# Kernel optimization log

Hardware: AMD Instinct MI355X
Metric: run time of the kernel (lower is better)

## Reference

```python
import jax, jax.numpy as jnp
import numpy as np

B, S, D = 2, 2048, 2048
H, HKV, DH = 16, 4, 128   # query heads, kv heads, head dim
N_REP = H // HKV
ROPE_BASE = 10000.0


def rotate_half(x):
    x1, x2 = x[..., : DH // 2], x[..., DH // 2 :]
    return jnp.concatenate((-x2, x1), axis=-1)


def rope_tables(seq_len, dtype=jnp.float32):
    inv_freq = 1.0 / (ROPE_BASE ** (jnp.arange(0, DH, 2, dtype=jnp.float32) / DH))
    t = jnp.arange(seq_len, dtype=jnp.float32)
    freqs = jnp.outer(t, inv_freq)                 # [S, DH/2]
    emb = jnp.concatenate((freqs, freqs), axis=-1)  # [S, DH]
    return jnp.cos(emb).astype(dtype), jnp.sin(emb).astype(dtype)


def setup_inputs() -> dict:
    key = jax.random.key(0)
    k1, k2, k3, k4, k5 = jax.random.split(key, 5)
    scale = 1.0 / np.sqrt(D)
    return {
        "hidden_states": jax.random.normal(k1, (B, S, D), dtype=jnp.float32),
        "position_ids": jnp.tile(jnp.arange(S, dtype=jnp.int32)[None, :], (B, 1)),
        "wq": jax.random.normal(k2, (D, H * DH), dtype=jnp.float32) * scale,
        "wk": jax.random.normal(k3, (D, HKV * DH), dtype=jnp.float32) * scale,
        "wv": jax.random.normal(k4, (D, HKV * DH), dtype=jnp.float32) * scale,
        "wo": jax.random.normal(k5, (H * DH, D), dtype=jnp.float32) * scale,
    }


def reference(hidden_states, position_ids, wq, wk, wv, wo):
    x = hidden_states
    b, s, _ = x.shape

    # QKV projections -> [B, H(kv), S, DH]
    q = (x @ wq).reshape(b, s, H, DH).transpose(0, 2, 1, 3)
    k = (x @ wk).reshape(b, s, HKV, DH).transpose(0, 2, 1, 3)
    v = (x @ wv).reshape(b, s, HKV, DH).transpose(0, 2, 1, 3)

    # Rotary position embedding
    cos_t, sin_t = rope_tables(s, x.dtype)
    cos = cos_t[position_ids][:, None, :, :]  # [B,1,S,DH]
    sin = sin_t[position_ids][:, None, :, :]
    q = q * cos + rotate_half(q) * sin
    k = k * cos + rotate_half(k) * sin

    # GQA: repeat KV heads to match query heads
    k = jnp.repeat(k, N_REP, axis=1)  # [B,H,S,DH]
    v = jnp.repeat(v, N_REP, axis=1)

    # Causal SDPA
    scores = jnp.einsum("bhqd,bhkd->bhqk", q, k) / jnp.sqrt(
        jnp.asarray(DH, x.dtype)
    )
    causal = jnp.tril(jnp.ones((s, s), dtype=bool))
    scores = jnp.where(causal[None, None], scores, jnp.asarray(-1e9, x.dtype))
    attn = jax.nn.softmax(scores, axis=-1)
    out = jnp.einsum("bhqk,bhkd->bhqd", attn, v)  # [B,H,S,DH]

    out = out.transpose(0, 2, 1, 3).reshape(b, s, H * DH)
    return out @ wo
```

## Files before the change

### kernel.cpp

```cpp
#include <hip/hip_runtime.h>
#include <cmath>

typedef unsigned short u16;
typedef float floatx4 __attribute__((ext_vector_type(4)));
typedef short short8 __attribute__((ext_vector_type(8)));
typedef short short4v __attribute__((ext_vector_type(4)));
typedef __bf16 bf16x8 __attribute__((ext_vector_type(8)));

#define GLOBAL_AS __attribute__((address_space(1)))
#define LDS_AS __attribute__((address_space(3)))

#define S_LEN 2048
#define D_MODEL 2048
#define NH 16
#define NKV 4
#define DHEAD 128
#define SM_SCALE 0.08838834764831843f
#define K2 (SM_SCALE * 1.4426950408889634f)

__device__ __forceinline__ u16 f2bf(float f) {
    unsigned int u = __builtin_bit_cast(unsigned int, f);
    u += 0x7fffu + ((u >> 16) & 1u);
    return (u16)(u >> 16);
}
__device__ __forceinline__ u16 f2bfr(float f) {
    unsigned int u = __builtin_bit_cast(unsigned int, f);
    return (u16)((u + 0x8000u) >> 16);
}
__device__ __forceinline__ float bf2f(u16 x) {
    unsigned int u = ((unsigned int)x) << 16;
    return __builtin_bit_cast(float, u);
}
__device__ __forceinline__ floatx4 zf4() {
    floatx4 z; z[0] = 0.f; z[1] = 0.f; z[2] = 0.f; z[3] = 0.f; return z;
}
__device__ __forceinline__ floatx4 mfma16(short8 a, short8 b, floatx4 c) {
    return __builtin_amdgcn_mfma_f32_16x16x32_bf16(
        __builtin_bit_cast(bf16x8, a), __builtin_bit_cast(bf16x8, b), c, 0, 0, 0);
}
__device__ __forceinline__ floatx4 mfma16k16(short4v a, short4v b, floatx4 c) {
    return __builtin_amdgcn_mfma_f32_16x16x16bf16_1k(a, b, c, 0, 0, 0);
}
__device__ __forceinline__ void async16(const u16* g, u16* l) {
    __builtin_amdgcn_global_load_lds((GLOBAL_AS void*)g, (LDS_AS void*)l, 16, 0, 0);
}

__global__ void cast_tables_kernel(const float4* __restrict__ in, ushort4* __restrict__ out,
                                   float* __restrict__ cs_tab, float* __restrict__ sn_tab) {
    int bid = blockIdx.x;
    if (bid < 8192) {
        int i = bid * 256 + threadIdx.x;
        float4 v = in[i];
        ushort4 o;
        o.x = f2bf(v.x); o.y = f2bf(v.y); o.z = f2bf(v.z); o.w = f2bf(v.w);
        out[i] = o;
    } else {
        int idx = (bid - 8192) * 256 + threadIdx.x;
        int p = idx >> 6, jj = idx & 63;
        double e = (double)(2 * jj) / 128.0;
        double invf = pow(10000.0, -e);
        float arg = (float)p * (float)invf;
        cs_tab[idx] = (float)cos((double)arg);
        sn_tab[idx] = (float)sin((double)arg);
    }
}

__global__ void transpose_all_kernel(const float* __restrict__ wq, const float* __restrict__ wk,
                                     const float* __restrict__ wv, const float* __restrict__ wo,
                                     u16* __restrict__ Wqkv, u16* __restrict__ Wo) {
    __shared__ float tile[32][33];
    int x = blockIdx.x;
    const float* in; u16* out; int C, bx;
    if (x < 64)      { in = wq; out = Wqkv;                     C = 2048; bx = x * 32; }
    else if (x < 80) { in = wk; out = Wqkv + (size_t)2048*2048; C = 512;  bx = (x - 64) * 32; }
    else if (x < 96) { in = wv; out = Wqkv + (size_t)2560*2048; C = 512;  bx = (x - 80) * 32; }
    else             { in = wo; out = Wo;                       C = 2048; bx = (x - 96) * 32; }
    const int R = 2048;
    int tx = threadIdx.x & 31, ty = threadIdx.x >> 5;
    int by = blockIdx.y * 32;
#pragma unroll
    for (int i = 0; i < 32; i += 8)
        tile[ty + i][tx] = in[(size_t)(by + ty + i) * C + bx + tx];
    __syncthreads();
#pragma unroll
    for (int i = 0; i < 32; i += 8)
        out[(size_t)(bx + ty + i) * R + by + tx] = f2bf(tile[tx][ty + i]);
}

__global__ void rope_k_kernel(u16* __restrict__ Kb, const int* __restrict__ pos,
                              const float4* __restrict__ cs_tab,
                              const float4* __restrict__ sn_tab) {
    int idx = blockIdx.x * 256 + threadIdx.x;
    int j4 = idx & 15;
    int s = (idx >> 4) & 2047;
    int r = idx >> 15;
    int hh = r & 3, b = r >> 2;
    int p = pos[b * S_LEN + s];
    float4 cs = cs_tab[p * 16 + j4];
    float4 sn = sn_tab[p * 16 + j4];
    u16* base = Kb + (((size_t)(b * NKV + hh)) * S_LEN + s) * DHEAD + j4 * 4;
    ushort4 a = *(const ushort4*)(base);
    ushort4 c = *(const ushort4*)(base + 64);
    ushort4 oa, oc;
    float x1, x2;
    x1 = bf2f(a.x); x2 = bf2f(c.x); oa.x = f2bf(x1 * cs.x - x2 * sn.x); oc.x = f2bf(x2 * cs.x + x1 * sn.x);
    x1 = bf2f(a.y); x2 = bf2f(c.y); oa.y = f2bf(x1 * cs.y - x2 * sn.y); oc.y = f2bf(x2 * cs.y + x1 * sn.y);
    x1 = bf2f(a.z); x2 = bf2f(c.z); oa.z = f2bf(x1 * cs.z - x2 * sn.z); oc.z = f2bf(x2 * cs.z + x1 * sn.z);
    x1 = bf2f(a.w); x2 = bf2f(c.w); oa.w = f2bf(x1 * cs.w - x2 * sn.w); oc.w = f2bf(x2 * cs.w + x1 * sn.w);
    *(ushort4*)(base) = oa;
    *(ushort4*)(base + 64) = oc;
}

template <int M_REP>
__device__ __forceinline__ void gemm_8ph(const u16* __restrict__ A,
                                         const u16* __restrict__ Bt, int K,
                                         u16* ldsA, u16* ldsB,
                                         floatx4 acc[M_REP][4]) {
    constexpr int BM = M_REP * 32;
    constexpr int ALOADS = BM / 64;
    const int t = threadIdx.x;
    const int lane = t & 63, wave = t >> 6;
    const int wr = wave >> 2, wc = wave & 3;
    const int lr = lane & 15, q = lane >> 4;
    const int swz = lr & 7;
    const int m0 = blockIdx.y * BM, n0 = blockIdx.x * 256;

#pragma unroll
    for (int r = 0; r < M_REP; ++r)
#pragma unroll
        for (int c = 0; c < 4; ++c) acc[r][c] = zf4();

    auto stageT = [&](int kt, int bs) {
#pragma unroll
        for (int i = 0; i < ALOADS; ++i) {
            int ci = i * 512 + t;
            int grow = ci >> 3;
            int kc = ((ci & 7) ^ (grow & 7)) << 3;
            async16(A + (size_t)(m0 + grow) * K + kt * 64 + kc,
                    ldsA + bs * (BM * 64) + (i * 512 + wave * 64) * 8);
        }
#pragma unroll
        for (int i = 0; i < 4; ++i) {
            int ci = i * 512 + t;
            int grow = ci >> 3;
            int kc = ((ci & 7) ^ (grow & 7)) << 3;
            async16(Bt + (size_t)(n0 + grow) * K + kt * 64 + kc,
                    ldsB + bs * (256 * 64) + (i * 512 + wave * 64) * 8);
        }
    };

    const int NT = K / 64;
    stageT(0, 0);

    for (int kt = 0; kt < NT; ++kt) {
        const int cur = kt & 1, nxt = cur ^ 1;
        const int kn = (kt + 1 < NT) ? kt + 1 : 0;
        const u16* la = ldsA + cur * (BM * 64);
        const u16* lb = ldsB + cur * (256 * 64);
        short8 af[M_REP / 2][2], bf[4][2];

        stageT(kn, nxt);
        if constexpr (M_REP == 8) asm volatile("s_waitcnt vmcnt(8)" ::: "memory");
        else                      asm volatile("s_waitcnt vmcnt(6)" ::: "memory");
        __builtin_amdgcn_s_barrier();
#pragma unroll
        for (int nf = 0; nf < 2; ++nf)
#pragma unroll
            for (int ks = 0; ks < 2; ++ks)
                bf[nf][ks] = *(const short8*)(lb + (wc * 64 + nf * 16 + lr) * 64 +
                                              (((ks * 4 + q) ^ swz) << 3));
#pragma unroll
        for (int mf = 0; mf < M_REP / 2; ++mf)
#pragma unroll
            for (int ks = 0; ks < 2; ++ks)
                af[mf][ks] = *(const short8*)(la + (wr * (M_REP * 16) + mf * 16 + lr) * 64 +
                                              (((ks * 4 + q) ^ swz) << 3));
        __builtin_amdgcn_s_barrier();
        __builtin_amdgcn_s_setprio(1);
#pragma unroll
        for (int mf = 0; mf < M_REP / 2; ++mf)
#pragma unroll
            for (int nf = 0; nf < 2; ++nf)
#pragma unroll
                for (int ks = 0; ks < 2; ++ks)
                    acc[mf][nf] = mfma16(af[mf][ks], bf[nf][ks], acc[mf][nf]);
        __builtin_amdgcn_s_setprio(0);
        __builtin_amdgcn_s_barrier();

#pragma unroll
        for (int nf = 0; nf < 2; ++nf)
#pragma unroll
            for (int ks = 0; ks < 2; ++ks)
                bf[2 + nf][ks] = *(const short8*)(lb + (wc * 64 + (2 + nf) * 16 + lr) * 64 +
                                                  (((ks * 4 + q) ^ swz) << 3));
        __builtin_amdgcn_s_barrier();
        __builtin_amdgcn_s_setprio(1);
#pragma unroll
        for (int mf = 0; mf < M_REP / 2; ++mf)
#pragma unroll
            for (int nf = 2; nf < 4; ++nf)
#pragma unroll
                for (int ks = 0; ks < 2; ++ks)
                    acc[mf][nf] = mfma16(af[mf][ks], bf[nf][ks], acc[mf][nf]);
        __builtin_amdgcn_s_setprio(0);
        __builtin_amdgcn_s_barrier();

#pragma unroll
        for (int mf = 0; mf < M_REP / 2; ++mf)
#pragma unroll
            for (int ks = 0; ks < 2; ++ks)
                af[mf][ks] = *(const short8*)(la + (wr * (M_REP * 16) +
                                              (M_REP / 2 + mf) * 16 + lr) * 64 +
                                              (((ks * 4 + q) ^ swz) << 3));
        __builtin_amdgcn_s_barrier();
        __builtin_amdgcn_s_setprio(1);
#pragma unroll
        for (int mf = 0; mf < M_REP / 2; ++mf)
#pragma unroll
            for (int nf = 0; nf < 2; ++nf)
#pragma unroll
                for (int ks = 0; ks < 2; ++ks)
                    acc[M_REP / 2 + mf][nf] =
                        mfma16(af[mf][ks], bf[nf][ks], acc[M_REP / 2 + mf][nf]);
        __builtin_amdgcn_s_setprio(0);
        __builtin_amdgcn_s_barrier();

        __builtin_amdgcn_s_setprio(1);
#pragma unroll
        for (int mf = 0; mf < M_REP / 2; ++mf)
#pragma unroll
            for (int nf = 2; nf < 4; ++nf)
#pragma unroll
                for (int ks = 0; ks < 2; ++ks)
                    acc[M_REP / 2 + mf][nf] =
                        mfma16(af[mf][ks], bf[nf][ks], acc[M_REP / 2 + mf][nf]);
        __builtin_amdgcn_s_setprio(0);
        __builtin_amdgcn_s_barrier();
    }
    asm volatile("s_waitcnt vmcnt(0)" ::: "memory");
}

__global__ __launch_bounds__(512, 1) void qkv_gemm_kernel(const u16* __restrict__ A,
                                                          const u16* __restrict__ Bt,
                                                          u16* __restrict__ Qb,
                                                          u16* __restrict__ Kb,
                                                          u16* __restrict__ Vt) {
    __shared__ u16 ldsA[2 * 256 * 64];
    __shared__ u16 ldsB[2 * 256 * 64];
    floatx4 acc[8][4];
    gemm_8ph<8>(A, Bt, D_MODEL, ldsA, ldsB, acc);

    const int t = threadIdx.x, lane = t & 63, wave = t >> 6;
    const int wr = wave >> 2, wc = wave & 3, lr = lane & 15, q = lane >> 4;
    const int m0 = blockIdx.y * 256 + wr * 128, n0 = blockIdx.x * 256 + wc * 64;
#pragma unroll
    for (int r = 0; r < 8; ++r)
#pragma unroll
        for (int c = 0; c < 4; ++c) {
            int gc = n0 + c * 16 + lr;
#pragma unroll
            for (int rr = 0; rr < 4; ++rr) {
                int grow = m0 + r * 16 + q * 4 + rr;
                int bb = grow >> 11, s = grow & 2047;
                u16 bv = f2bf(acc[r][c][rr]);
                int d = gc & 127;
                if (gc < 2048) {
                    int hh = gc >> 7;
                    Qb[(((size_t)(bb * NH + hh)) * S_LEN + s) * DHEAD + d] = bv;
                } else if (gc < 2560) {
                    int hh = (gc - 2048) >> 7;
                    Kb[(((size_t)(bb * NKV + hh)) * S_LEN + s) * DHEAD + d] = bv;
                } else {
                    int hh = (gc - 2560) >> 7;
                    int s2 = s ^ ((d & 8) >> 1);
                    Vt[(((size_t)(bb * NKV + hh)) * DHEAD + d) * S_LEN + s2] = bv;
                }
            }
        }
}

__global__ __launch_bounds__(512, 1) void out_gemm_kernel(const u16* __restrict__ A,
                                                          const u16* __restrict__ Bt,
                                                          float* __restrict__ out) {
    __shared__ u16 ldsA[2 * 128 * 64];
    __shared__ u16 ldsB[2 * 256 * 64];
    floatx4 acc[4][4];
    gemm_8ph<4>(A, Bt, D_MODEL, ldsA, ldsB, acc);

    const int t = threadIdx.x, lane = t & 63, wave = t >> 6;
    const int wr = wave >> 2, wc = wave & 3, lr = lane & 15, q = lane >> 4;
    const int m0 = blockIdx.y * 128 + wr * 64, n0 = blockIdx.x * 256 + wc * 64;
#pragma unroll
    for (int r = 0; r < 4; ++r)
#pragma unroll
        for (int c = 0; c < 4; ++c) {
            int gc = n0 + c * 16 + lr;
#pragma unroll
            for (int rr = 0; rr < 4; ++rr) {
                int grow = m0 + r * 16 + q * 4 + rr;
                out[(size_t)grow * D_MODEL + gc] = acc[r][c][rr];
            }
        }
}

__global__ __launch_bounds__(256, 2) void fa_kernel(const u16* __restrict__ Qb,
                                                    const u16* __restrict__ Kb,
                                                    const u16* __restrict__ Vt,
                                                    u16* __restrict__ Ob,
                                                    const int* __restrict__ pos,
                                                    const float4* __restrict__ cs_tab,
                                                    const float4* __restrict__ sn_tab) {
    __shared__ u16 ldsK[2][64 * 128];
    __shared__ u16 ldsV[2][128 * 64];

    const int t = threadIdx.x, lane = t & 63, wave = t >> 6;
    const int lr = lane & 15, q = lane >> 4;
    const int swz = lr & 7;

    const int bid = blockIdx.x;
    const int bh = bid >> 4, p = bid & 15;
    const int qt0 = p, qt1 = 31 - p;
    const int b = bh >> 4, h = bh & 15;
    const int kvh = h >> 2;

    const u16* Kp = Kb + (size_t)(b * NKV + kvh) * S_LEN * DHEAD;
    const u16* Vp = Vt + (size_t)(b * NKV + kvh) * DHEAD * S_LEN;

    short8 qf0[4], qf1[4];
    auto load_rope_q = [&](int qt, short8 (&qf)[4]) {
        const u16* Qp = Qb + ((size_t)((b * NH + h) * S_LEN) + qt * 64 + wave * 16) * DHEAD;
#pragma unroll
        for (int kk = 0; kk < 4; ++kk)
            qf[kk] = *(const short8*)(Qp + (size_t)lr * DHEAD + kk * 32 + q * 8);
        const int srow = qt * 64 + wave * 16 + lr;
        const int pp = pos[b * S_LEN + srow];
#pragma unroll
        for (int kk = 0; kk < 2; ++kk)
#pragma unroll
            for (int h4 = 0; h4 < 2; ++h4) {
                float4 cs = cs_tab[pp * 16 + kk * 8 + q * 2 + h4];
                float4 sn = sn_tab[pp * 16 + kk * 8 + q * 2 + h4];
#pragma unroll
                for (int e = 0; e < 4; ++e) {
                    float cc = (&cs.x)[e], ss = (&sn.x)[e];
                    int ei = h4 * 4 + e;
                    float x1 = bf2f((u16)qf[kk][ei]);
                    float x2 = bf2f((u16)qf[kk + 2][ei]);
                    qf[kk][ei]     = (short)f2bf(x1 * cc - x2 * ss);
                    qf[kk + 2][ei] = (short)f2bf(x2 * cc + x1 * ss);
                }
            }
    };
    load_rope_q(qt0, qf0);
    load_rope_q(qt1, qf1);

    auto stage = [&](int kt, int bs) {
#pragma unroll
        for (int i = 0; i < 4; ++i) {
            int ci = i * 256 + t;
            int krow = ci >> 4, kc = ((ci & 15) ^ ((ci >> 4) & 7)) << 3;
            async16(Kp + (size_t)(kt * 64 + krow) * DHEAD + kc,
                    &ldsK[bs][(i * 256 + wave * 64) * 8]);
            int dh = ci >> 3, vc = ((ci & 7) ^ ((ci >> 3) & 7)) << 3;
            async16(Vp + (size_t)dh * S_LEN + kt * 64 + vc,
                    &ldsV[bs][(i * 256 + wave * 64) * 8]);
        }
    };

    floatx4 accO[8];
    float m_i, l_i;

    auto do_tile = [&](int kt, int qt_c, const short8 (&qfc)[4], int bs) {
        floatx4 sc[4];
        __builtin_amdgcn_s_setprio(1);
#pragma unroll
        for (int c = 0; c < 4; ++c) {
            sc[c] = zf4();
#pragma unroll
            for (int kk = 0; kk < 4; ++kk) {
                short8 kfr = *(const short8*)(&ldsK[bs][(c * 16 + lr) * DHEAD +
                                              (((kk * 4 + q) ^ swz) << 3)]);
                sc[c] = mfma16(kfr, qfc[kk], sc[c]);
            }
        }
        __builtin_amdgcn_s_setprio(0);

        if (kt == qt_c) {
            const int qrow = wave * 16 + lr;
#pragma unroll
            for (int c = 0; c < 4; ++c)
#pragma unroll
                for (int rr = 0; rr < 4; ++rr)
                    if (c * 16 + q * 4 + rr > qrow) sc[c][rr] = -3e38f;
        }

        float mx = -3e38f;
#pragma unroll
        for (int c = 0; c < 4; ++c)
#pragma unroll
            for (int rr = 0; rr < 4; ++rr) mx = fmaxf(mx, sc[c][rr]);
        mx = fmaxf(mx, __shfl_xor(mx, 16));
        mx = fmaxf(mx, __shfl_xor(mx, 32));
        float mnew = fmaxf(m_i, mx);
        float mk = mnew * K2;
        bool anyup = __any(mnew > m_i);
        float rs = 0.f;
#pragma unroll
        for (int c = 0; c < 4; ++c)
#pragma unroll
            for (int rr = 0; rr < 4; ++rr) {
                float pe = __builtin_amdgcn_exp2f(fmaf(sc[c][rr], K2, -mk));
                sc[c][rr] = pe;
                rs += pe;
            }
        rs += __shfl_xor(rs, 16);
        rs += __shfl_xor(rs, 32);
        if (anyup) {
            float alpha = __builtin_amdgcn_exp2f(fmaf(m_i, K2, -mk));
            l_i = l_i * alpha + rs;
#pragma unroll
            for (int d = 0; d < 8; ++d) accO[d] *= alpha;
        } else {
            l_i += rs;
        }
        m_i = mnew;

        short4v pb[4];
#pragma unroll
        for (int c = 0; c < 4; ++c) {
            pb[c][0] = (short)f2bfr(sc[c][0]);
            pb[c][1] = (short)f2bfr(sc[c][1]);
            pb[c][2] = (short)f2bfr(sc[c][2]);
            pb[c][3] = (short)f2bfr(sc[c][3]);
        }

        __builtin_amdgcn_s_setprio(1);
#pragma unroll
        for (int ks = 0; ks < 4; ++ks)
#pragma unroll
            for (int d = 0; d < 8; ++d) {
                short4v vf = *(const short4v*)(&ldsV[bs][(d * 16 + lr) * 64 +
                                               (((ks * 2 + (q >> 1)) ^ swz) << 3) +
                                               (((q ^ (lr >> 3)) & 1) << 2)]);
                accO[d] = mfma16k16(vf, pb[ks], accO[d]);
            }
        __builtin_amdgcn_s_setprio(0);
    };

    auto epilogue = [&](int qt_c) {
        const int tok = qt_c * 64 + wave * 16 + lr;
        const float inv = 1.0f / l_i;
        u16* orow = Ob + ((size_t)(b * S_LEN + tok)) * (NH * DHEAD) + h * DHEAD + q * 4;
#pragma unroll
        for (int d = 0; d < 8; ++d) {
            ushort4 o;
            o.x = f2bf(accO[d][0] * inv);
            o.y = f2bf(accO[d][1] * inv);
            o.z = f2bf(accO[d][2] * inv);
            o.w = f2bf(accO[d][3] * inv);
            *(ushort4*)(orow + d * 16) = o;
        }
    };

#pragma unroll
    for (int d = 0; d < 8; ++d) accO[d] = zf4();
    m_i = -3e38f; l_i = 0.f;

    int cur = 0;
    stage(0, 0);
    __syncthreads();

    for (int kt = 0; kt <= qt0; ++kt) {
        int nxt = cur ^ 1;
        int nk = (kt < qt0) ? kt + 1 : 0;
        stage(nk, nxt);
        do_tile(kt, qt0, qf0, cur);
        __syncthreads();
        cur = nxt;
    }
    epilogue(qt0);
#pragma unroll
    for (int d = 0; d < 8; ++d) accO[d] = zf4();
    m_i = -3e38f; l_i = 0.f;

    for (int kt = 0; kt <= qt1; ++kt) {
        int nxt = cur ^ 1;
        if (kt < qt1) stage(kt + 1, nxt);
        do_tile(kt, qt1, qf1, cur);
        __syncthreads();
        cur = nxt;
    }
    epilogue(qt1);
}

extern "C" void kernel_launch(void* const* d_in, const int* in_sizes, int n_in,
                              void* d_out, int out_size, void* d_ws, size_t ws_size,
                              hipStream_t stream) {
    const float* X  = (const float*)d_in[0];
    const int* pos  = (const int*)d_in[1];
    const float* wq = (const float*)d_in[2];
    const float* wk = (const float*)d_in[3];
    const float* wv = (const float*)d_in[4];
    const float* wo = (const float*)d_in[5];
    float* out = (float*)d_out;

    char* w = (char*)d_ws;
    u16* Xbf    = (u16*)(w);
    u16* Wqkv   = (u16*)(w + 16777216);
    u16* Wo     = (u16*)(w + 29360128);
    u16* Qb     = (u16*)(w + 37748736);
    u16* Kb     = (u16*)(w + 54525952);
    u16* Vt     = (u16*)(w + 58720256);
    u16* Ob     = (u16*)(w + 62914560);
    float* cst  = (float*)(w + 79691776);
    float* snt  = (float*)(w + 80216064);

    cast_tables_kernel<<<8704, 256, 0, stream>>>((const float4*)X, (ushort4*)Xbf, cst, snt);
    transpose_all_kernel<<<dim3(160, 64), 256, 0, stream>>>(wq, wk, wv, wo, Wqkv, Wo);
    qkv_gemm_kernel<<<dim3(12, 16), 512, 0, stream>>>(Xbf, Wqkv, Qb, Kb, Vt);
    rope_k_kernel<<<1024, 256, 0, stream>>>(Kb, pos, (const float4*)cst, (const float4*)snt);
    fa_kernel<<<512, 256, 0, stream>>>(Qb, Kb, Vt, Ob, pos, (const float4*)cst, (const float4*)snt);
    out_gemm_kernel<<<dim3(8, 32), 512, 0, stream>>>(Ob, Wo, out);
}
```

Baseline: 340.6 us.

## Fuse prologue kernels, remap GEMM tiles per XCD, restructure small-tile GEMM phases

Merges the input cast/rope-table kernel and the weight transpose kernel into a single prologue launch. Switches the QKV and output GEMMs to 1D grids whose block-to-tile mapping groups tiles sharing A rows onto the same XCD, to improve L2 reuse. For the M_REP=4 GEMM, the inner loop loads all B fragments at once and uses two compute phases instead of four, reducing barriers at the cost of more live registers.

```diff
diff --git a/kernel.cpp b/kernel.cpp
--- a/kernel.cpp
+++ b/kernel.cpp
@@ -45,16 +45,22 @@
     __builtin_amdgcn_global_load_lds((GLOBAL_AS void*)g, (LDS_AS void*)l, 16, 0, 0);
 }
 
-__global__ void cast_tables_kernel(const float4* __restrict__ in, ushort4* __restrict__ out,
-                                   float* __restrict__ cs_tab, float* __restrict__ sn_tab) {
+__global__ void prologue_kernel(const float4* __restrict__ Xin, ushort4* __restrict__ Xout,
+                                float* __restrict__ cs_tab, float* __restrict__ sn_tab,
+                                const float* __restrict__ wq, const float* __restrict__ wk,
+                                const float* __restrict__ wv, const float* __restrict__ wo,
+                                u16* __restrict__ Wqkv, u16* __restrict__ Wo) {
+    __shared__ float tile[32][33];
     int bid = blockIdx.x;
     if (bid < 8192) {
         int i = bid * 256 + threadIdx.x;
-        float4 v = in[i];
+        float4 v = Xin[i];
         ushort4 o;
         o.x = f2bf(v.x); o.y = f2bf(v.y); o.z = f2bf(v.z); o.w = f2bf(v.w);
-        out[i] = o;
-    } else {
+        Xout[i] = o;
+        return;
+    }
+    if (bid < 8704) {
         int idx = (bid - 8192) * 256 + threadIdx.x;
         int p = idx >> 6, jj = idx & 63;
         double e = (double)(2 * jj) / 128.0;
@@ -62,14 +68,10 @@
         float arg = (float)p * (float)invf;
         cs_tab[idx] = (float)cos((double)arg);
         sn_tab[idx] = (float)sin((double)arg);
+        return;
     }
-}
-
-__global__ void transpose_all_kernel(const float* __restrict__ wq, const float* __restrict__ wk,
-                                     const float* __restrict__ wv, const float* __restrict__ wo,
-                                     u16* __restrict__ Wqkv, u16* __restrict__ Wo) {
-    __shared__ float tile[32][33];
-    int x = blockIdx.x;
+    int tb = bid - 8704;
+    int x = tb % 160, y = tb / 160;
     const float* in; u16* out; int C, bx;
     if (x < 64)      { in = wq; out = Wqkv;                     C = 2048; bx = x * 32; }
     else if (x < 80) { in = wk; out = Wqkv + (size_t)2048*2048; C = 512;  bx = (x - 64) * 32; }
@@ -77,7 +79,7 @@
     else             { in = wo; out = Wo;                       C = 2048; bx = (x - 96) * 32; }
     const int R = 2048;
     int tx = threadIdx.x & 31, ty = threadIdx.x >> 5;
-    int by = blockIdx.y * 32;
+    int by = y * 32;
 #pragma unroll
     for (int i = 0; i < 32; i += 8)
         tile[ty + i][tx] = in[(size_t)(by + ty + i) * C + bx + tx];
@@ -112,10 +114,11 @@
 }
 
 template <int M_REP>
-__device__ __forceinline__ void gemm_8ph(const u16* __restrict__ A,
-                                         const u16* __restrict__ Bt, int K,
-                                         u16* ldsA, u16* ldsB,
-                                         floatx4 acc[M_REP][4]) {
+__device__ __forceinline__ void gemm_ph(const u16* __restrict__ A,
+                                        const u16* __restrict__ Bt, int K,
+                                        u16* ldsA, u16* ldsB,
+                                        floatx4 acc[M_REP][4],
+                                        int m0, int n0) {
     constexpr int BM = M_REP * 32;
     constexpr int ALOADS = BM / 64;
     const int t = threadIdx.x;
@@ -123,7 +126,6 @@
     const int wr = wave >> 2, wc = wave & 3;
     const int lr = lane & 15, q = lane >> 4;
     const int swz = lr & 7;
-    const int m0 = blockIdx.y * BM, n0 = blockIdx.x * 256;
 
 #pragma unroll
     for (int r = 0; r < M_REP; ++r)
@@ -157,85 +159,124 @@
         const int kn = (kt + 1 < NT) ? kt + 1 : 0;
         const u16* la = ldsA + cur * (BM * 64);
         const u16* lb = ldsB + cur * (256 * 64);
-        short8 af[M_REP / 2][2], bf[4][2];
 
         stageT(kn, nxt);
         if constexpr (M_REP == 8) asm volatile("s_waitcnt vmcnt(8)" ::: "memory");
         else                      asm volatile("s_waitcnt vmcnt(6)" ::: "memory");
         __builtin_amdgcn_s_barrier();
-#pragma unroll
-        for (int nf = 0; nf < 2; ++nf)
-#pragma unroll
-            for (int ks = 0; ks < 2; ++ks)
-                bf[nf][ks] = *(const short8*)(lb + (wc * 64 + nf * 16 + lr) * 64 +
-                                              (((ks * 4 + q) ^ swz) << 3));
-#pragma unroll
-        for (int mf = 0; mf < M_REP / 2; ++mf)
-#pragma unroll
-            for (int ks = 0; ks < 2; ++ks)
-                af[mf][ks] = *(const short8*)(la + (wr * (M_REP * 16) + mf * 16 + lr) * 64 +
-                                              (((ks * 4 + q) ^ swz) << 3));
-        __builtin_amdgcn_s_barrier();
-        __builtin_amdgcn_s_setprio(1);
-#pragma unroll
-        for (int mf = 0; mf < M_REP / 2; ++mf)
+
+        if constexpr (M_REP == 8) {
+            short8 af[4][2], bf[4][2];
 #pragma unroll
             for (int nf = 0; nf < 2; ++nf)
 #pragma unroll
                 for (int ks = 0; ks < 2; ++ks)
-                    acc[mf][nf] = mfma16(af[mf][ks], bf[nf][ks], acc[mf][nf]);
-        __builtin_amdgcn_s_setprio(0);
-        __builtin_amdgcn_s_barrier();
-
-#pragma unroll
-        for (int nf = 0; nf < 2; ++nf)
-#pragma unroll
-            for (int ks = 0; ks < 2; ++ks)
-                bf[2 + nf][ks] = *(const short8*)(lb + (wc * 64 + (2 + nf) * 16 + lr) * 64 +
+                    bf[nf][ks] = *(const short8*)(lb + (wc * 64 + nf * 16 + lr) * 64 +
                                                   (((ks * 4 + q) ^ swz) << 3));
-        __builtin_amdgcn_s_barrier();
-        __builtin_amdgcn_s_setprio(1);
-#pragma unroll
-        for (int mf = 0; mf < M_REP / 2; ++mf)
-#pragma unroll
-            for (int nf = 2; nf < 4; ++nf)
-#pragma unroll
-                for (int ks = 0; ks < 2; ++ks)
-                    acc[mf][nf] = mfma16(af[mf][ks], bf[nf][ks], acc[mf][nf]);
-        __builtin_amdgcn_s_setprio(0);
-        __builtin_amdgcn_s_barrier();
-
-#pragma unroll
-        for (int mf = 0; mf < M_REP / 2; ++mf)
-#pragma unroll
-            for (int ks = 0; ks < 2; ++ks)
-                af[mf][ks] = *(const short8*)(la + (wr * (M_REP * 16) +
-                                              (M_REP / 2 + mf) * 16 + lr) * 64 +
-                                              (((ks * 4 + q) ^ swz) << 3));
-        __builtin_amdgcn_s_barrier();
-        __builtin_amdgcn_s_setprio(1);
-#pragma unroll
-        for (int mf = 0; mf < M_REP / 2; ++mf)
+#pragma unroll
+            for (int mf = 0; mf < 4; ++mf)
+#pragma unroll
+                for (int ks = 0; ks < 2; ++ks)
+                    af[mf][ks] = *(const short8*)(la + (wr * 128 + mf * 16 + lr) * 64 +
+                                                  (((ks * 4 + q) ^ swz) << 3));
+            __builtin_amdgcn_s_barrier();
+            __builtin_amdgcn_s_setprio(1);
+#pragma unroll
+            for (int mf = 0; mf < 4; ++mf)
+#pragma unroll
+                for (int nf = 0; nf < 2; ++nf)
+#pragma unroll
+                    for (int ks = 0; ks < 2; ++ks)
+                        acc[mf][nf] = mfma16(af[mf][ks], bf[nf][ks], acc[mf][nf]);
+            __builtin_amdgcn_s_setprio(0);
+            __builtin_amdgcn_s_barrier();
 #pragma unroll
             for (int nf = 0; nf < 2; ++nf)
 #pragma unroll
                 for (int ks = 0; ks < 2; ++ks)
-                    acc[M_REP / 2 + mf][nf] =
-                        mfma16(af[mf][ks], bf[nf][ks], acc[M_REP / 2 + mf][nf]);
-        __builtin_amdgcn_s_setprio(0);
-        __builtin_amdgcn_s_barrier();
-
-        __builtin_amdgcn_s_setprio(1);
-#pragma unroll
-        for (int mf = 0; mf < M_REP / 2; ++mf)
-#pragma unroll
-            for (int nf = 2; nf < 4; ++nf)
-#pragma unroll
-                for (int ks = 0; ks < 2; ++ks)
-                    acc[M_REP / 2 + mf][nf] =
-                        mfma16(af[mf][ks], bf[nf][ks], acc[M_REP / 2 + mf][nf]);
-        __builtin_amdgcn_s_setprio(0);
-        __builtin_amdgcn_s_barrier();
+                    bf[2 + nf][ks] = *(const short8*)(lb + (wc * 64 + (2 + nf) * 16 + lr) * 64 +
+                                                      (((ks * 4 + q) ^ swz) << 3));
+            __builtin_amdgcn_s_barrier();
+            __builtin_amdgcn_s_setprio(1);
+#pragma unroll
+            for (int mf = 0; mf < 4; ++mf)
+#pragma unroll
+                for (int nf = 2; nf < 4; ++nf)
+#pragma unroll
+                    for (int ks = 0; ks < 2; ++ks)
+                        acc[mf][nf] = mfma16(af[mf][ks], bf[nf][ks], acc[mf][nf]);
+            __builtin_amdgcn_s_setprio(0);
+            __builtin_amdgcn_s_barrier();
+#pragma unroll
+            for (int mf = 0; mf < 4; ++mf)
+#pragma unroll
+                for (int ks = 0; ks < 2; ++ks)
+                    af[mf][ks] = *(const short8*)(la + (wr * 128 + (4 + mf) * 16 + lr) * 64 +
+                                                  (((ks * 4 + q) ^ swz) << 3));
+            __builtin_amdgcn_s_barrier();
+            __builtin_amdgcn_s_setprio(1);
+#pragma unroll
+            for (int mf = 0; mf < 4; ++mf)
+#pragma unroll
+                for (int nf = 0; nf < 2; ++nf)
+#pragma unroll
+                    for (int ks = 0; ks < 2; ++ks)
+                        acc[4 + mf][nf] = mfma16(af[mf][ks], bf[nf][ks], acc[4 + mf][nf]);
+            __builtin_amdgcn_s_setprio(0);
+            __builtin_amdgcn_s_barrier();
+            __builtin_amdgcn_s_setprio(1);
+#pragma unroll
+            for (int mf = 0; mf < 4; ++mf)
+#pragma unroll
+                for (int nf = 2; nf < 4; ++nf)
+#pragma unroll
+                    for (int ks = 0; ks < 2; ++ks)
+                        acc[4 + mf][nf] = mfma16(af[mf][ks], bf[nf][ks], acc[4 + mf][nf]);
+            __builtin_amdgcn_s_setprio(0);
+            __builtin_amdgcn_s_barrier();
+        } else {
+            short8 af[2][2], bf[4][2];
+#pragma unroll
+            for (int nf = 0; nf < 4; ++nf)
+#pragma unroll
+                for (int ks = 0; ks < 2; ++ks)
+                    bf[nf][ks] = *(const short8*)(lb + (wc * 64 + nf * 16 + lr) * 64 +
+                                                  (((ks * 4 + q) ^ swz) << 3));
+#pragma unroll
+            for (int mf = 0; mf < 2; ++mf)
+#pragma unroll
+                for (int ks = 0; ks < 2; ++ks)
+                    af[mf][ks] = *(const short8*)(la + (wr * 64 + mf * 16 + lr) * 64 +
+                                                  (((ks * 4 + q) ^ swz) << 3));
+            __builtin_amdgcn_s_barrier();
+            __builtin_amdgcn_s_setprio(1);
+#pragma unroll
+            for (int mf = 0; mf < 2; ++mf)
+#pragma unroll
+                for (int nf = 0; nf < 4; ++nf)
+#pragma unroll
+                    for (int ks = 0; ks < 2; ++ks)
+                        acc[mf][nf] = mfma16(af[mf][ks], bf[nf][ks], acc[mf][nf]);
+            __builtin_amdgcn_s_setprio(0);
+            __builtin_amdgcn_s_barrier();
+#pragma unroll
+            for (int mf = 0; mf < 2; ++mf)
+#pragma unroll
+                for (int ks = 0; ks < 2; ++ks)
+                    af[mf][ks] = *(const short8*)(la + (wr * 64 + (2 + mf) * 16 + lr) * 64 +
+                                                  (((ks * 4 + q) ^ swz) << 3));
+            __builtin_amdgcn_s_barrier();
+            __builtin_amdgcn_s_setprio(1);
+#pragma unroll
+            for (int mf = 0; mf < 2; ++mf)
+#pragma unroll
+                for (int nf = 0; nf < 4; ++nf)
+#pragma unroll
+                    for (int ks = 0; ks < 2; ++ks)
+                        acc[2 + mf][nf] = mfma16(af[mf][ks], bf[nf][ks], acc[2 + mf][nf]);
+            __builtin_amdgcn_s_setprio(0);
+            __builtin_amdgcn_s_barrier();
+        }
     }
     asm volatile("s_waitcnt vmcnt(0)" ::: "memory");
 }
@@ -247,20 +288,24 @@
                                                           u16* __restrict__ Vt) {
     __shared__ u16 ldsA[2 * 256 * 64];
     __shared__ u16 ldsB[2 * 256 * 64];
+    const int xcd = blockIdx.x & 7, slot = blockIdx.x >> 3;
+    const int by = 2 * xcd + (slot >= 12), bx = slot % 12;
+    const int m0 = by * 256, n0 = bx * 256;
+
     floatx4 acc[8][4];
-    gemm_8ph<8>(A, Bt, D_MODEL, ldsA, ldsB, acc);
+    gemm_ph<8>(A, Bt, D_MODEL, ldsA, ldsB, acc, m0, n0);
 
     const int t = threadIdx.x, lane = t & 63, wave = t >> 6;
     const int wr = wave >> 2, wc = wave & 3, lr = lane & 15, q = lane >> 4;
-    const int m0 = blockIdx.y * 256 + wr * 128, n0 = blockIdx.x * 256 + wc * 64;
+    const int em0 = m0 + wr * 128, en0 = n0 + wc * 64;
 #pragma unroll
     for (int r = 0; r < 8; ++r)
 #pragma unroll
         for (int c = 0; c < 4; ++c) {
-            int gc = n0 + c * 16 + lr;
+            int gc = en0 + c * 16 + lr;
 #pragma unroll
             for (int rr = 0; rr < 4; ++rr) {
-                int grow = m0 + r * 16 + q * 4 + rr;
+                int grow = em0 + r * 16 + q * 4 + rr;
                 int bb = grow >> 11, s = grow & 2047;
                 u16 bv = f2bf(acc[r][c][rr]);
                 int d = gc & 127;
@@ -284,20 +329,24 @@
                                                           float* __restrict__ out) {
     __shared__ u16 ldsA[2 * 128 * 64];
     __shared__ u16 ldsB[2 * 256 * 64];
+    const int xcd = blockIdx.x & 7, slot = blockIdx.x >> 3;
+    const int by = 4 * xcd + (slot >> 3), bx = slot & 7;
+    const int m0 = by * 128, n0 = bx * 256;
+
     floatx4 acc[4][4];
-    gemm_8ph<4>(A, Bt, D_MODEL, ldsA, ldsB, acc);
+    gemm_ph<4>(A, Bt, D_MODEL, ldsA, ldsB, acc, m0, n0);
 
     const int t = threadIdx.x, lane = t & 63, wave = t >> 6;
     const int wr = wave >> 2, wc = wave & 3, lr = lane & 15, q = lane >> 4;
-    const int m0 = blockIdx.y * 128 + wr * 64, n0 = blockIdx.x * 256 + wc * 64;
+    const int em0 = m0 + wr * 64, en0 = n0 + wc * 64;
 #pragma unroll
     for (int r = 0; r < 4; ++r)
 #pragma unroll
         for (int c = 0; c < 4; ++c) {
-            int gc = n0 + c * 16 + lr;
+            int gc = en0 + c * 16 + lr;
 #pragma unroll
             for (int rr = 0; rr < 4; ++rr) {
-                int grow = m0 + r * 16 + q * 4 + rr;
+                int grow = em0 + r * 16 + q * 4 + rr;
                 out[(size_t)grow * D_MODEL + gc] = acc[r][c][rr];
             }
         }
@@ -515,10 +564,10 @@
     float* cst  = (float*)(w + 79691776);
     float* snt  = (float*)(w + 80216064);
 
-    cast_tables_kernel<<<8704, 256, 0, stream>>>((const float4*)X, (ushort4*)Xbf, cst, snt);
-    transpose_all_kernel<<<dim3(160, 64), 256, 0, stream>>>(wq, wk, wv, wo, Wqkv, Wo);
-    qkv_gemm_kernel<<<dim3(12, 16), 512, 0, stream>>>(Xbf, Wqkv, Qb, Kb, Vt);
+    prologue_kernel<<<18944, 256, 0, stream>>>((const float4*)X, (ushort4*)Xbf, cst, snt,
+                                               wq, wk, wv, wo, Wqkv, Wo);
+    qkv_gemm_kernel<<<192, 512, 0, stream>>>(Xbf, Wqkv, Qb, Kb, Vt);
     rope_k_kernel<<<1024, 256, 0, stream>>>(Kb, pos, (const float4*)cst, (const float4*)snt);
     fa_kernel<<<512, 256, 0, stream>>>(Qb, Kb, Vt, Ob, pos, (const float4*)cst, (const float4*)snt);
-    out_gemm_kernel<<<dim3(8, 32), 512, 0, stream>>>(Ob, Wo, out);
-}
+    out_gemm_kernel<<<256, 512, 0, stream>>>(Ob, Wo, out);
+}
```

New measurement: 329.5 us. 3.2% less time.
